# Kernel optimization log

Measured on AMD Instinct MI355X. Metric: run time of the kernel, lower is better.

The kernel has to match this reference:

```python
import jax, jax.numpy as jnp
import numpy as np

N_NODES = 100000
T = 1024        # number of visits / hyperedges (GRU sequence length)
IN = 128        # in_channel
HID = 256       # hid_channel


def setup_inputs() -> dict:
    key = jax.random.key(0)
    ks = jax.random.split(key, 7)
    X = jax.random.normal(ks[0], (N_NODES, IN), dtype=jnp.float32)
    H = jax.random.uniform(ks[1], (N_NODES, T), dtype=jnp.float32)
    s = 1.0 / np.sqrt(HID)  # torch default GRU init scale
    w_ih = jax.random.uniform(ks[2], (3 * HID, IN), jnp.float32, -s, s)
    w_hh = jax.random.uniform(ks[3], (3 * HID, HID), jnp.float32, -s, s)
    b_ih = jax.random.uniform(ks[4], (3 * HID,), jnp.float32, -s, s)
    b_hh = jax.random.uniform(ks[5], (3 * HID,), jnp.float32, -s, s)
    w_attn = jax.random.uniform(ks[6], (HID,), jnp.float32, -s, s)
    return {"X": X, "H": H, "w_ih": w_ih, "w_hh": w_hh,
            "b_ih": b_ih, "b_hh": b_hh, "w_attn": w_attn}


def _gru(visit_emb, w_ih, w_hh, b_ih, b_hh):
    # Precompute input-side gates for all timesteps: [T, 3H]
    gx = visit_emb @ w_ih.T + b_ih

    def step(h, gx_t):
        gh = h @ w_hh.T + b_hh
        xr, xz, xn = jnp.split(gx_t, 3)
        hr, hz, hn = jnp.split(gh, 3)
        r = jax.nn.sigmoid(xr + hr)
        z = jax.nn.sigmoid(xz + hz)
        n = jnp.tanh(xn + r * hn)
        h_new = (1.0 - z) * n + z * h
        return h_new, h_new

    h0 = jnp.zeros((HID,), visit_emb.dtype)
    _, hs = jax.lax.scan(step, h0, gx)
    return hs  # [T, HID]


def reference(X, H, w_ih, w_hh, b_ih, b_hh, w_attn):
    # visit_emb = H.T @ X : [T, IN]
    visit_emb = H.T @ X
    hs = _gru(visit_emb, w_ih, w_hh, b_ih, b_hh)          # [T, HID]
    alpha = jax.nn.softmax(hs @ w_attn)                    # [T]
    # sum(diag(alpha) @ hs, 0) == alpha-weighted sum of hidden states
    return alpha @ hs                                      # [HID]
```

## Files before the change

kernel.cpp:

```cpp
#include <hip/hip_runtime.h>
#include <hip/hip_bf16.h>
#include <hip/hip_fp16.h>

#define T_STEPS 1024
#define INC 128
#define HIDC 256
#define G3 768
#define NN 100000
#define KSPLIT 32
#define NCHUNK 3125

typedef _Float16 h2 __attribute__((ext_vector_type(2)));

__device__ __forceinline__ float fdot2f(h2 a, h2 b, float c){
#if __has_builtin(__builtin_amdgcn_fdot2)
  return __builtin_amdgcn_fdot2(a, b, c, false);
#else
  return c + (float)a[0]*(float)b[0] + (float)a[1]*(float)b[1];
#endif
}

__global__ __launch_bounds__(256) void k_phase1(const float* __restrict__ X,
                                                const float* __restrict__ Hm,
                                                float* __restrict__ part){
  const int tt = blockIdx.x;
  const int ks = blockIdx.y;
  const int t0 = tt * 64;
  const int nbeg = ks * NCHUNK;
  const int nend = nbeg + NCHUNK;
  __shared__ float Hs[8][64];
  __shared__ float Xs[8][128];
  const int tid = threadIdx.x;
  const int tx = tid & 31;
  const int ty = tid >> 5;
  float acc[8][4];
  #pragma unroll
  for (int r = 0; r < 8; r++){ acc[r][0]=0.f; acc[r][1]=0.f; acc[r][2]=0.f; acc[r][3]=0.f; }

  for (int n0 = nbeg; n0 < nend; n0 += 8){
    {
      int n = n0 + ty;
      float2 hv = {0.f, 0.f};
      float4 xv = {0.f, 0.f, 0.f, 0.f};
      if (n < nend){
        hv = *(const float2*)(Hm + (size_t)n * T_STEPS + t0 + tx * 2);
        xv = *(const float4*)(X  + (size_t)n * INC + tx * 4);
      }
      *(float2*)&Hs[ty][tx * 2] = hv;
      *(float4*)&Xs[ty][tx * 4] = xv;
    }
    __syncthreads();
    #pragma unroll
    for (int i = 0; i < 8; i++){
      float4 xr = *(const float4*)&Xs[i][tx * 4];
      float hr[8];
      *(float4*)&hr[0] = *(const float4*)&Hs[i][ty * 8];
      *(float4*)&hr[4] = *(const float4*)&Hs[i][ty * 8 + 4];
      #pragma unroll
      for (int r = 0; r < 8; r++){
        acc[r][0] += hr[r] * xr.x;
        acc[r][1] += hr[r] * xr.y;
        acc[r][2] += hr[r] * xr.z;
        acc[r][3] += hr[r] * xr.w;
      }
    }
    __syncthreads();
  }
  #pragma unroll
  for (int r = 0; r < 8; r++){
    size_t o = ((size_t)ks * T_STEPS + t0 + ty * 8 + r) * INC + tx * 4;
    float4 v = make_float4(acc[r][0], acc[r][1], acc[r][2], acc[r][3]);
    *(float4*)&part[o] = v;
  }
}

__global__ __launch_bounds__(256) void k_reduce(const float* __restrict__ part,
                                                float* __restrict__ ve){
  int idx = blockIdx.x * 256 + threadIdx.x;
  float s = 0.f;
  #pragma unroll
  for (int ks = 0; ks < KSPLIT; ks++) s += part[(size_t)ks * (T_STEPS * INC) + idx];
  ve[idx] = s;
}

__global__ __launch_bounds__(768) void k_gx(const float* __restrict__ ve,
                                            const float* __restrict__ w_ih,
                                            const float* __restrict__ b_ih,
                                            float* __restrict__ gx){
  const int t = blockIdx.x;
  const int j = threadIdx.x;
  __shared__ float4 v4[32];
  if (j < 32) v4[j] = *(const float4*)(ve + (size_t)t * INC + j * 4);
  __syncthreads();
  const float4* wr = (const float4*)(w_ih + (size_t)j * INC);
  float a0 = b_ih[j], a1 = 0.f, a2 = 0.f, a3 = 0.f;
  #pragma unroll
  for (int q = 0; q < 32; q++){
    float4 w = wr[q]; float4 v = v4[q];
    a0 += w.x * v.x; a1 += w.y * v.y; a2 += w.z * v.z; a3 += w.w * v.w;
  }
  gx[(size_t)t * G3 + j] = (a0 + a1) + (a2 + a3);
}

__global__ __launch_bounds__(768) void k_gru(const float* __restrict__ w_hh,
                                             const float* __restrict__ b_hh,
                                             const float* __restrict__ gx,
                                             float* __restrict__ hs){
  const int tid = threadIdx.x;
  __shared__ float4 h16v[HIDC / 8];
  __shared__ float h32[HIDC];
  __shared__ float rbuf[HIDC];
  __shared__ float zbuf[HIDC];
  __shared__ float nbuf[HIDC];

  h2 w[128];
  {
    const float4* wr = (const float4*)(w_hh + (size_t)tid * HIDC);
    #pragma unroll
    for (int q = 0; q < 64; q++){
      float4 v = wr[q];
      h2 p0; p0[0] = (_Float16)v.x; p0[1] = (_Float16)v.y;
      h2 p1; p1[0] = (_Float16)v.z; p1[1] = (_Float16)v.w;
      w[2 * q]     = p0;
      w[2 * q + 1] = p1;
    }
  }
  const float bias = b_hh[tid];
  if (tid < HIDC){ h32[tid] = 0.f; ((_Float16*)h16v)[tid] = (_Float16)0.f; }
  __syncthreads();

  float xg_pref = gx[tid];
  for (int t = 0; t < T_STEPS; t++){
    float xg = xg_pref;
    int tn = (t + 1 < T_STEPS) ? (t + 1) : t;
    xg_pref = gx[(size_t)tn * G3 + tid];

    float a0 = 0.f, a1 = 0.f, a2 = 0.f, a3 = 0.f;
    #pragma unroll
    for (int q = 0; q < 32; q++){
      float4 hv = h16v[q];
      h2 b0 = __builtin_bit_cast(h2, hv.x);
      h2 b1 = __builtin_bit_cast(h2, hv.y);
      h2 b2 = __builtin_bit_cast(h2, hv.z);
      h2 b3 = __builtin_bit_cast(h2, hv.w);
      a0 = fdot2f(w[4 * q + 0], b0, a0);
      a1 = fdot2f(w[4 * q + 1], b1, a1);
      a2 = fdot2f(w[4 * q + 2], b2, a2);
      a3 = fdot2f(w[4 * q + 3], b3, a3);
    }
    const float acc = (a0 + a1) + (a2 + a3) + bias;

    if (tid < HIDC){
      rbuf[tid] = 1.f / (1.f + __expf(-(xg + acc)));
    } else if (tid < 2 * HIDC){
      zbuf[tid - HIDC] = 1.f / (1.f + __expf(-(xg + acc)));
    }
    __syncthreads();
    if (tid >= 2 * HIDC){
      int i = tid - 2 * HIDC;
      float pre = xg + rbuf[i] * acc;
      float ax = fabsf(pre);
      float e = __expf(-2.f * ax);
      float th = (1.f - e) / (1.f + e);
      nbuf[i] = copysignf(th, pre);
    }
    __syncthreads();
    if (tid < HIDC){
      float z = zbuf[tid];
      float hn = (1.f - z) * nbuf[tid] + z * h32[tid];
      h32[tid] = hn;
      ((_Float16*)h16v)[tid] = (_Float16)hn;
      hs[(size_t)t * HIDC + tid] = hn;
    }
    __syncthreads();
  }
}

__global__ __launch_bounds__(64) void k_logits(const float* __restrict__ hs,
                                               const float* __restrict__ w_attn,
                                               float* __restrict__ logits){
  int t = blockIdx.x;
  int l = threadIdx.x;
  float4 hv = *(const float4*)(hs + (size_t)t * HIDC + l * 4);
  float4 wv = *(const float4*)(w_attn + l * 4);
  float p = hv.x * wv.x + hv.y * wv.y + hv.z * wv.z + hv.w * wv.w;
  #pragma unroll
  for (int o = 32; o > 0; o >>= 1) p += __shfl_down(p, o);
  if (l == 0) logits[t] = p;
}

__global__ __launch_bounds__(1024) void k_attn(const float* __restrict__ logits,
                                               const float* __restrict__ hs,
                                               float* __restrict__ out){
  __shared__ float sm[1024];
  __shared__ float al[1024];
  __shared__ float ps[4][HIDC];
  int tid = threadIdx.x;
  float lg = logits[tid];
  sm[tid] = lg; __syncthreads();
  for (int s = 512; s > 0; s >>= 1){
    if (tid < s) sm[tid] = fmaxf(sm[tid], sm[tid + s]);
    __syncthreads();
  }
  float mx = sm[0]; __syncthreads();
  float e = __expf(lg - mx);
  sm[tid] = e; __syncthreads();
  for (int s = 512; s > 0; s >>= 1){
    if (tid < s) sm[tid] += sm[tid + s];
    __syncthreads();
  }
  float inv = 1.f / sm[0];
  al[tid] = e * inv;
  __syncthreads();
  int c = tid & 255; int tq = tid >> 8;
  float acc = 0.f;
  for (int t = tq; t < T_STEPS; t += 4) acc += al[t] * hs[(size_t)t * HIDC + c];
  ps[tq][c] = acc; __syncthreads();
  if (tid < HIDC) out[tid] = (ps[0][tid] + ps[1][tid]) + (ps[2][tid] + ps[3][tid]);
}

extern "C" void kernel_launch(void* const* d_in, const int* in_sizes, int n_in,
                              void* d_out, int out_size, void* d_ws, size_t ws_size,
                              hipStream_t stream){
  const float* X      = (const float*)d_in[0];
  const float* Hm     = (const float*)d_in[1];
  const float* w_ih   = (const float*)d_in[2];
  const float* w_hh   = (const float*)d_in[3];
  const float* b_ih   = (const float*)d_in[4];
  const float* b_hh   = (const float*)d_in[5];
  const float* w_attn = (const float*)d_in[6];
  float* out = (float*)d_out;

  float* ws     = (float*)d_ws;
  float* part   = ws;
  float* ve     = part + 4194304;
  float* gx     = ve + 131072;
  float* hs     = gx + 786432;
  float* logits = hs + 262144;

  k_phase1<<<dim3(16, 32), 256, 0, stream>>>(X, Hm, part);
  k_reduce<<<512, 256, 0, stream>>>(part, ve);
  k_gx<<<1024, 768, 0, stream>>>(ve, w_ih, b_ih, gx);
  k_gru<<<1, 768, 0, stream>>>(w_hh, b_hh, gx, hs);
  k_logits<<<1024, 64, 0, stream>>>(hs, w_attn, logits);
  k_attn<<<1, 1024, 0, stream>>>(logits, hs, out);
}
```

Measured before the change: 2.439 ms.

## Use MFMA for GRU recurrence with double-buffered hidden state and retile phase1

Replaces the per-thread fdot2 GRU matvec with 16x16x32 fp16 MFMA instructions across 16 wavefronts. Each lane keeps its slice of w_hh in registers, the hidden state is double-buffered in LDS so each step needs one barrier instead of three, and the r/z/n gates are computed in the same thread. The r and z biases are folded into the precomputed input gates, which are interleaved per unit for a single vector load. The H^T X phase is retiled to 512 threads, 128 timesteps per block and a skewed LDS layout. The risks are extra MFMA latency on the serial path and a prefetch at t+1 that reads past the last step into padded workspace.

After: 2.304 ms. -5.6%, faster.

```diff
diff --git a/kernel.cpp b/kernel.cpp
--- a/kernel.cpp
+++ b/kernel.cpp
@@ -1,6 +1,8 @@
 #include <hip/hip_runtime.h>
-#include <hip/hip_bf16.h>
 #include <hip/hip_fp16.h>
+
+typedef _Float16 half8 __attribute__((ext_vector_type(8)));
+typedef float f32x4 __attribute__((ext_vector_type(4)));
 
 #define T_STEPS 1024
 #define INC 128
@@ -9,68 +11,64 @@
 #define NN 100000
 #define KSPLIT 32
 #define NCHUNK 3125
-
-typedef _Float16 h2 __attribute__((ext_vector_type(2)));
-
-__device__ __forceinline__ float fdot2f(h2 a, h2 b, float c){
-#if __has_builtin(__builtin_amdgcn_fdot2)
-  return __builtin_amdgcn_fdot2(a, b, c, false);
-#else
-  return c + (float)a[0]*(float)b[0] + (float)a[1]*(float)b[1];
-#endif
-}
-
-__global__ __launch_bounds__(256) void k_phase1(const float* __restrict__ X,
+#define XS_STRIDE 144
+
+__global__ __launch_bounds__(512) void k_phase1(const float* __restrict__ X,
                                                 const float* __restrict__ Hm,
                                                 float* __restrict__ part){
   const int tt = blockIdx.x;
   const int ks = blockIdx.y;
-  const int t0 = tt * 64;
+  const int t0 = tt * 128;
   const int nbeg = ks * NCHUNK;
   const int nend = nbeg + NCHUNK;
-  __shared__ float Hs[8][64];
-  __shared__ float Xs[8][128];
+  __shared__ float Hs[16][128];
+  __shared__ float Xs[16 * XS_STRIDE];
   const int tid = threadIdx.x;
-  const int tx = tid & 31;
-  const int ty = tid >> 5;
-  float acc[8][4];
-  #pragma unroll
-  for (int r = 0; r < 8; r++){ acc[r][0]=0.f; acc[r][1]=0.f; acc[r][2]=0.f; acc[r][3]=0.f; }
-
-  for (int n0 = nbeg; n0 < nend; n0 += 8){
+  const int tx = tid & 15;
+  const int ty = tid >> 4;
+  const int sr = tid >> 5;
+  const int sc = tid & 31;
+  const int xskew = tx * 8 + (tx >> 2) * 4;
+
+  float acc[4][8];
+  #pragma unroll
+  for (int r = 0; r < 4; r++)
+    #pragma unroll
+    for (int q = 0; q < 8; q++) acc[r][q] = 0.f;
+
+  for (int n0 = nbeg; n0 < nend; n0 += 16){
+    int n = n0 + sr;
+    float4 hv = {0.f,0.f,0.f,0.f}, xv = {0.f,0.f,0.f,0.f};
+    if (n < nend){
+      hv = *(const float4*)(Hm + (size_t)n * T_STEPS + t0 + sc * 4);
+      xv = *(const float4*)(X  + (size_t)n * INC + sc * 4);
+    }
+    __syncthreads();
+    *(float4*)&Hs[sr][sc * 4] = hv;
     {
-      int n = n0 + ty;
-      float2 hv = {0.f, 0.f};
-      float4 xv = {0.f, 0.f, 0.f, 0.f};
-      if (n < nend){
-        hv = *(const float2*)(Hm + (size_t)n * T_STEPS + t0 + tx * 2);
-        xv = *(const float4*)(X  + (size_t)n * INC + tx * 4);
-      }
-      *(float2*)&Hs[ty][tx * 2] = hv;
-      *(float4*)&Xs[ty][tx * 4] = xv;
-    }
-    __syncthreads();
-    #pragma unroll
-    for (int i = 0; i < 8; i++){
-      float4 xr = *(const float4*)&Xs[i][tx * 4];
-      float hr[8];
-      *(float4*)&hr[0] = *(const float4*)&Hs[i][ty * 8];
-      *(float4*)&hr[4] = *(const float4*)&Hs[i][ty * 8 + 4];
+      int g = sc >> 1, hf = sc & 1;
+      *(float4*)&Xs[sr * XS_STRIDE + g * 8 + (g >> 2) * 4 + hf * 4] = xv;
+    }
+    __syncthreads();
+    #pragma unroll
+    for (int i = 0; i < 16; i++){
+      float4 h4 = *(const float4*)&Hs[i][ty * 4];
+      float4 x0 = *(const float4*)&Xs[i * XS_STRIDE + xskew];
+      float4 x1 = *(const float4*)&Xs[i * XS_STRIDE + xskew + 4];
+      float xr[8] = {x0.x,x0.y,x0.z,x0.w,x1.x,x1.y,x1.z,x1.w};
+      float hr[4] = {h4.x,h4.y,h4.z,h4.w};
       #pragma unroll
-      for (int r = 0; r < 8; r++){
-        acc[r][0] += hr[r] * xr.x;
-        acc[r][1] += hr[r] * xr.y;
-        acc[r][2] += hr[r] * xr.z;
-        acc[r][3] += hr[r] * xr.w;
-      }
-    }
-    __syncthreads();
-  }
-  #pragma unroll
-  for (int r = 0; r < 8; r++){
-    size_t o = ((size_t)ks * T_STEPS + t0 + ty * 8 + r) * INC + tx * 4;
-    float4 v = make_float4(acc[r][0], acc[r][1], acc[r][2], acc[r][3]);
-    *(float4*)&part[o] = v;
+      for (int r = 0; r < 4; r++)
+        #pragma unroll
+        for (int q = 0; q < 8; q++)
+          acc[r][q] += hr[r] * xr[q];
+    }
+  }
+  #pragma unroll
+  for (int r = 0; r < 4; r++){
+    size_t o = ((size_t)ks * T_STEPS + t0 + ty * 4 + r) * INC + tx * 8;
+    *(float4*)&part[o]     = make_float4(acc[r][0], acc[r][1], acc[r][2], acc[r][3]);
+    *(float4*)&part[o + 4] = make_float4(acc[r][4], acc[r][5], acc[r][6], acc[r][7]);
   }
 }
 
@@ -86,92 +84,84 @@
 __global__ __launch_bounds__(768) void k_gx(const float* __restrict__ ve,
                                             const float* __restrict__ w_ih,
                                             const float* __restrict__ b_ih,
-                                            float* __restrict__ gx){
+                                            const float* __restrict__ b_hh,
+                                            float* __restrict__ gxq){
   const int t = blockIdx.x;
   const int j = threadIdx.x;
   __shared__ float4 v4[32];
   if (j < 32) v4[j] = *(const float4*)(ve + (size_t)t * INC + j * 4);
   __syncthreads();
   const float4* wr = (const float4*)(w_ih + (size_t)j * INC);
-  float a0 = b_ih[j], a1 = 0.f, a2 = 0.f, a3 = 0.f;
+  float a0 = 0.f, a1 = 0.f, a2 = 0.f, a3 = 0.f;
   #pragma unroll
   for (int q = 0; q < 32; q++){
     float4 w = wr[q]; float4 v = v4[q];
     a0 += w.x * v.x; a1 += w.y * v.y; a2 += w.z * v.z; a3 += w.w * v.w;
   }
-  gx[(size_t)t * G3 + j] = (a0 + a1) + (a2 + a3);
-}
-
-__global__ __launch_bounds__(768) void k_gru(const float* __restrict__ w_hh,
-                                             const float* __restrict__ b_hh,
-                                             const float* __restrict__ gx,
-                                             float* __restrict__ hs){
-  const int tid = threadIdx.x;
-  __shared__ float4 h16v[HIDC / 8];
-  __shared__ float h32[HIDC];
-  __shared__ float rbuf[HIDC];
-  __shared__ float zbuf[HIDC];
-  __shared__ float nbuf[HIDC];
-
-  h2 w[128];
-  {
-    const float4* wr = (const float4*)(w_hh + (size_t)tid * HIDC);
-    #pragma unroll
-    for (int q = 0; q < 64; q++){
-      float4 v = wr[q];
-      h2 p0; p0[0] = (_Float16)v.x; p0[1] = (_Float16)v.y;
-      h2 p1; p1[0] = (_Float16)v.z; p1[1] = (_Float16)v.w;
-      w[2 * q]     = p0;
-      w[2 * q + 1] = p1;
-    }
-  }
-  const float bias = b_hh[tid];
-  if (tid < HIDC){ h32[tid] = 0.f; ((_Float16*)h16v)[tid] = (_Float16)0.f; }
+  float bias = b_ih[j] + (j < 512 ? b_hh[j] : 0.f);
+  gxq[(size_t)t * 1024 + (j & 255) * 4 + (j >> 8)] = (a0 + a1) + (a2 + a3) + bias;
+}
+
+__global__ __launch_bounds__(1024) void k_gru(const float* __restrict__ w_hh,
+                                              const float* __restrict__ b_hh,
+                                              const float* __restrict__ gxq,
+                                              float* __restrict__ hs){
+  const int tid  = threadIdx.x;
+  const int w    = tid >> 6;
+  const int l    = tid & 63;
+  const int col  = l & 15;
+  const int quad = l >> 4;
+  const int unit = w * 16 + col;
+
+  __shared__ _Float16 hbuf[2][256];
+
+  half8 Bf[3][8];
+  #pragma unroll
+  for (int g = 0; g < 3; g++){
+    const float* wr = w_hh + (size_t)(g * 256 + unit) * HIDC + quad * 8;
+    #pragma unroll
+    for (int c = 0; c < 8; c++){
+      float4 v0 = *(const float4*)(wr + c * 32);
+      float4 v1 = *(const float4*)(wr + c * 32 + 4);
+      half8 b;
+      b[0]=(_Float16)v0.x; b[1]=(_Float16)v0.y; b[2]=(_Float16)v0.z; b[3]=(_Float16)v0.w;
+      b[4]=(_Float16)v1.x; b[5]=(_Float16)v1.y; b[6]=(_Float16)v1.z; b[7]=(_Float16)v1.w;
+      Bf[g][c] = b;
+    }
+  }
+  const float bn = b_hh[512 + unit];
+  float hprev = 0.f;
+  if (tid < 256) hbuf[0][tid] = (_Float16)0.f;
   __syncthreads();
 
-  float xg_pref = gx[tid];
+  f32x4 gq = *(const f32x4*)(gxq + (size_t)unit * 4);
+
   for (int t = 0; t < T_STEPS; t++){
-    float xg = xg_pref;
-    int tn = (t + 1 < T_STEPS) ? (t + 1) : t;
-    xg_pref = gx[(size_t)tn * G3 + tid];
-
-    float a0 = 0.f, a1 = 0.f, a2 = 0.f, a3 = 0.f;
-    #pragma unroll
-    for (int q = 0; q < 32; q++){
-      float4 hv = h16v[q];
-      h2 b0 = __builtin_bit_cast(h2, hv.x);
-      h2 b1 = __builtin_bit_cast(h2, hv.y);
-      h2 b2 = __builtin_bit_cast(h2, hv.z);
-      h2 b3 = __builtin_bit_cast(h2, hv.w);
-      a0 = fdot2f(w[4 * q + 0], b0, a0);
-      a1 = fdot2f(w[4 * q + 1], b1, a1);
-      a2 = fdot2f(w[4 * q + 2], b2, a2);
-      a3 = fdot2f(w[4 * q + 3], b3, a3);
-    }
-    const float acc = (a0 + a1) + (a2 + a3) + bias;
-
-    if (tid < HIDC){
-      rbuf[tid] = 1.f / (1.f + __expf(-(xg + acc)));
-    } else if (tid < 2 * HIDC){
-      zbuf[tid - HIDC] = 1.f / (1.f + __expf(-(xg + acc)));
-    }
-    __syncthreads();
-    if (tid >= 2 * HIDC){
-      int i = tid - 2 * HIDC;
-      float pre = xg + rbuf[i] * acc;
-      float ax = fabsf(pre);
-      float e = __expf(-2.f * ax);
-      float th = (1.f - e) / (1.f + e);
-      nbuf[i] = copysignf(th, pre);
-    }
-    __syncthreads();
-    if (tid < HIDC){
-      float z = zbuf[tid];
-      float hn = (1.f - z) * nbuf[tid] + z * h32[tid];
-      h32[tid] = hn;
-      ((_Float16*)h16v)[tid] = (_Float16)hn;
-      hs[(size_t)t * HIDC + tid] = hn;
-    }
+    f32x4 dr = {0.f,0.f,0.f,0.f}, dz = {0.f,0.f,0.f,0.f}, dn = {0.f,0.f,0.f,0.f};
+    const _Float16* hb = hbuf[t & 1];
+    #pragma unroll
+    for (int c = 0; c < 8; c++){
+      half8 a = *(const half8*)(hb + c * 32 + quad * 8);
+      dr = __builtin_amdgcn_mfma_f32_16x16x32_f16(a, Bf[0][c], dr, 0, 0, 0);
+      dz = __builtin_amdgcn_mfma_f32_16x16x32_f16(a, Bf[1][c], dz, 0, 0, 0);
+      dn = __builtin_amdgcn_mfma_f32_16x16x32_f16(a, Bf[2][c], dn, 0, 0, 0);
+    }
+    f32x4 gq_n = *(const f32x4*)(gxq + (size_t)(t + 1) * 1024 + unit * 4);
+
+    float r = 1.f / (1.f + __expf(-(gq[0] + dr[0])));
+    float z = 1.f / (1.f + __expf(-(gq[1] + dz[0])));
+    float pre = gq[2] + r * (dn[0] + bn);
+    float ax = fabsf(pre);
+    float e = __expf(-2.f * ax);
+    float th = (1.f - e) / (1.f + e);
+    float n = copysignf(th, pre);
+    float hnew = n + z * (hprev - n);
+    hprev = hnew;
+    if (quad == 0){
+      hbuf[(t + 1) & 1][unit] = (_Float16)hnew;
+      hs[(size_t)t * HIDC + unit] = hnew;
+    }
+    gq = gq_n;
     __syncthreads();
   }
 }
@@ -234,14 +224,14 @@
   float* ws     = (float*)d_ws;
   float* part   = ws;
   float* ve     = part + 4194304;
-  float* gx     = ve + 131072;
-  float* hs     = gx + 786432;
+  float* gxq    = ve + 131072;
+  float* hs     = gxq + 1049600;
   float* logits = hs + 262144;
 
-  k_phase1<<<dim3(16, 32), 256, 0, stream>>>(X, Hm, part);
+  k_phase1<<<dim3(8, 32), 512, 0, stream>>>(X, Hm, part);
   k_reduce<<<512, 256, 0, stream>>>(part, ve);
-  k_gx<<<1024, 768, 0, stream>>>(ve, w_ih, b_ih, gx);
-  k_gru<<<1, 768, 0, stream>>>(w_hh, b_hh, gx, hs);
+  k_gx<<<1024, 768, 0, stream>>>(ve, w_ih, b_ih, b_hh, gxq);
+  k_gru<<<1, 1024, 0, stream>>>(w_hh, b_hh, gxq, hs);
   k_logits<<<1024, 64, 0, stream>>>(hs, w_attn, logits);
   k_attn<<<1, 1024, 0, stream>>>(logits, hs, out);
 }
```
